# Optimization experiments

Hardware: AMD Instinct MI355X
Metric: run time of the kernel (lower is better)

The kernel has to match this reference:

```python
import jax, jax.numpy as jnp
import numpy as np

UNITS = 512
EPS = 1e-6

def setup_inputs() -> dict:
    key = jax.random.key(0)
    x = jax.random.normal(key, (262144, UNITS), dtype=jnp.float32)
    return {"x": x}

def reference(x):
    d = x.shape[1]
    # Gram matrix with diagonal jitter: [d, d]
    g = x.T @ x + jnp.eye(d, dtype=x.dtype) * EPS
    L = jnp.linalg.cholesky(g)  # lower triangular [d, d]
    # inv(L) via triangular solve (same math as tf.linalg.inv on L)
    L_inv = jax.scipy.linalg.solve_triangular(L, jnp.eye(d, dtype=x.dtype), lower=True)
    ortho_weights = L_inv.T * jnp.sqrt(jnp.float32(UNITS))
    return x @ ortho_weights
```

## Files before the change

### kernel.cpp

```cpp
#include <hip/hip_runtime.h>


#define EPSJ 1e-6f
#define SQRTD 22.627416997969522f

typedef short bf16x8 __attribute__((ext_vector_type(8)));
typedef float f32x4 __attribute__((ext_vector_type(4)));

__device__ __forceinline__ unsigned short f2bf(float f) {
  unsigned u = __float_as_uint(f);
  unsigned r = u + 0x7fffu + ((u >> 16) & 1u);
  return (unsigned short)(r >> 16);
}

__device__ __forceinline__ int swz(int row, int slot) {
  return slot ^ ((row ^ (row >> 3)) & 7);
}

__device__ __forceinline__ float wred(float s) {
  s += __shfl_xor(s, 1);  s += __shfl_xor(s, 2);  s += __shfl_xor(s, 4);
  s += __shfl_xor(s, 8);  s += __shfl_xor(s, 16); s += __shfl_xor(s, 32);
  return s;
}

__global__ __launch_bounds__(512, 2) void gram_partial(
    const float* __restrict__ X, float* __restrict__ part, int nchunk) {
  __shared__ unsigned short As[256 * 64];
  __shared__ unsigned short Bs[256 * 64];
  const int b = blockIdx.x;
  const int pos = b % 3;
  const int chunk = b / 3;
  const int CR = 262144 / nchunk;
  const long r0 = (long)chunk * CR;
  const int ca = (pos == 1) ? 256 : 0;
  const int cb = (pos == 0) ? 0 : 256;
  const bool diag = (pos != 2);
  const int t = threadIdx.x, lane = t & 63, w = t >> 6;
  const int wr = w >> 2, wc = w & 3;

  f32x4 acc[8][4];
  const f32x4 zf = {0.f, 0.f, 0.f, 0.f};
  #pragma unroll
  for (int a = 0; a < 8; ++a)
    #pragma unroll
    for (int bb = 0; bb < 4; ++bb) acc[a][bb] = zf;

  const int c_oct = t & 31, msub = t >> 5;

  for (int ks = 0; ks < CR; ks += 64) {
    #pragma unroll
    for (int it = 0; it < 4; ++it) {
      int m = msub + 16 * it;
      long row = r0 + ks + m;
      const float4* sa = (const float4*)(X + row * 512 + ca + c_oct * 8);
      float4 a0 = sa[0], a1 = sa[1];
      {
        float v[8] = {a0.x, a0.y, a0.z, a0.w, a1.x, a1.y, a1.z, a1.w};
        #pragma unroll
        for (int s = 0; s < 8; ++s) {
          int c = c_oct * 8 + s;
          int off = c * 128 + ((2 * m) ^ (((c ^ (c >> 3)) & 7) << 4));
          *(unsigned short*)((char*)As + off) = f2bf(v[s]);
        }
      }
      if (!diag) {
        const float4* sb = (const float4*)(X + row * 512 + cb + c_oct * 8);
        float4 b0 = sb[0], b1 = sb[1];
        float v[8] = {b0.x, b0.y, b0.z, b0.w, b1.x, b1.y, b1.z, b1.w};
        #pragma unroll
        for (int s = 0; s < 8; ++s) {
          int c = c_oct * 8 + s;
          int off = c * 128 + ((2 * m) ^ (((c ^ (c >> 3)) & 7) << 4));
          *(unsigned short*)((char*)Bs + off) = f2bf(v[s]);
        }
      }
    }
    __syncthreads();
    const unsigned short* Bp = diag ? As : Bs;
    #pragma unroll
    for (int kk = 0; kk < 2; ++kk) {
      bf16x8 af[8], bfr[4];
      #pragma unroll
      for (int fm = 0; fm < 8; ++fm) {
        int row = wr * 128 + fm * 16 + (lane & 15);
        int slot = swz(row, kk * 4 + (lane >> 4));
        af[fm] = *(const bf16x8*)((const char*)As + row * 128 + slot * 16);
      }
      #pragma unroll
      for (int fn = 0; fn < 4; ++fn) {
        int row = wc * 64 + fn * 16 + (lane & 15);
        int slot = swz(row, kk * 4 + (lane >> 4));
        bfr[fn] = *(const bf16x8*)((const char*)Bp + row * 128 + slot * 16);
      }
      #pragma unroll
      for (int fm = 0; fm < 8; ++fm)
        #pragma unroll
        for (int fn = 0; fn < 4; ++fn)
          acc[fm][fn] = __builtin_amdgcn_mfma_f32_16x16x32_bf16(
              af[fm], bfr[fn], acc[fm][fn], 0, 0, 0);
    }
    __syncthreads();
  }
  float* out = part + (long)b * 65536;
  #pragma unroll
  for (int fm = 0; fm < 8; ++fm)
    #pragma unroll
    for (int fn = 0; fn < 4; ++fn)
      #pragma unroll
      for (int j = 0; j < 4; ++j) {
        int i  = wr * 128 + fm * 16 + (lane >> 4) * 4 + j;
        int jj = wc * 64 + fn * 16 + (lane & 15);
        out[i * 256 + jj] = acc[fm][fn][j];
      }
}

__global__ void gram_reduce(const float* __restrict__ part,
                            float* __restrict__ G, int nchunk) {
  int idx = blockIdx.x * 256 + threadIdx.x;
  int pos = idx >> 16;
  int e = idx & 65535;
  float s = 0.f;
  for (int ch = 0; ch < nchunk; ++ch)
    s += part[(long)(ch * 3 + pos) * 65536 + e];
  int i = e >> 8, j = e & 255;
  if (pos == 0) {
    G[i * 512 + j] = s;
  } else if (pos == 1) {
    G[(256 + i) * 512 + 256 + j] = s;
  } else {
    G[i * 512 + 256 + j] = s;
    G[(256 + j) * 512 + i] = s;
  }
}

__global__ void chol_diag(float* __restrict__ G, int c0) {
  __shared__ float P[128][129];
  int t = threadIdx.x;
  for (int idx = t; idx < 128 * 128; idx += 512) {
    int i = idx >> 7, j = idx & 127;
    float v = G[(long)(c0 + i) * 512 + c0 + j];
    if (i == j) v += EPSJ;
    P[i][j] = v;
  }
  __syncthreads();
  int lane = t & 63, w = t >> 6;
  for (int sp = 0; sp < 4; ++sp) {
    int b0 = sp * 32;
    if (w == 0) {
      float r[32];
      #pragma unroll
      for (int k = 0; k < 32; ++k) r[k] = (lane < 32) ? P[b0 + lane][b0 + k] : 0.f;
      #pragma unroll
      for (int j = 0; j < 32; ++j) {
        float d = sqrtf(__shfl(r[j], j));
        if (lane == j) r[j] = d;
        else if (lane > j && lane < 32) r[j] = r[j] / d;
        float rj = r[j];
        #pragma unroll
        for (int k = j + 1; k < 32; ++k) {
          float Lkj = __shfl(rj, k);
          if (lane > j && lane < 32) r[k] -= rj * Lkj;
        }
      }
      #pragma unroll
      for (int k = 0; k < 32; ++k) if (lane < 32) P[b0 + lane][b0 + k] = r[k];
    }
    __syncthreads();
    int nb = 128 - (b0 + 32);
    if (nb > 0) {
      if (t < nb) {
        int rr = b0 + 32 + t;
        float x[32];
        #pragma unroll
        for (int j = 0; j < 32; ++j) x[j] = P[rr][b0 + j];
        #pragma unroll
        for (int j = 0; j < 32; ++j) {
          float xj = x[j] / P[b0 + j][b0 + j];
          x[j] = xj;
          #pragma unroll
          for (int k2 = j + 1; k2 < 32; ++k2) x[k2] -= xj * P[b0 + k2][b0 + j];
        }
        #pragma unroll
        for (int j = 0; j < 32; ++j) P[rr][b0 + j] = x[j];
      }
      __syncthreads();
      int total = nb * nb;
      for (int idx = t; idx < total; idx += 512) {
        int i = b0 + 32 + idx / nb, k = b0 + 32 + idx % nb;
        float s = P[i][k];
        #pragma unroll
        for (int j = 0; j < 32; ++j) s -= P[i][b0 + j] * P[k][b0 + j];
        P[i][k] = s;
      }
      __syncthreads();
    }
  }
  for (int idx = t; idx < 128 * 128; idx += 512) {
    int i = idx >> 7, j = idx & 127;
    G[(long)(c0 + i) * 512 + c0 + j] = P[i][j];
  }
}

__global__ void chol_solve(float* __restrict__ G, int p) {
  int c0 = 128 * p;
  int row0 = c0 + 128;
  int w = threadIdx.x >> 6, lane = threadIdx.x & 63;
  long r = row0 + blockIdx.x * 4 + w;
  float x[2];
  x[0] = G[r * 512 + c0 + lane];
  x[1] = G[r * 512 + c0 + 64 + lane];
  #pragma unroll
  for (int q = 0; q < 2; ++q) {
    for (int ii = 0; ii < 64; ++ii) {
      int i = q * 64 + ii;
      const float* Lrow = G + (long)(c0 + i) * 512 + c0;
      float s = 0.f;
      if (q == 1) s += x[0] * Lrow[lane];
      s += (lane < ii) ? x[q] * Lrow[q * 64 + lane] : 0.f;
      s = wred(s);
      float ai = __shfl(x[q], ii);
      float xi = (ai - s) / Lrow[i];
      if (lane == ii) x[q] = xi;
    }
  }
  G[r * 512 + c0 + lane] = x[0];
  G[r * 512 + c0 + 64 + lane] = x[1];
}

__global__ void chol_syrk(float* __restrict__ G, int t0) {
  int id = blockIdx.x;
  int ti = 0;
  while ((ti + 1) * (ti + 2) / 2 <= id) ++ti;
  int tj = id - ti * (ti + 1) / 2;
  __shared__ float As2[64][130], Bs2[64][130];
  int t = threadIdx.x;
  int c0 = t0 - 128;
  for (int idx = t; idx < 64 * 128; idx += 256) {
    int i = idx >> 7, j = idx & 127;
    As2[i][j] = G[(long)(t0 + 64 * ti + i) * 512 + c0 + j];
    Bs2[i][j] = G[(long)(t0 + 64 * tj + i) * 512 + c0 + j];
  }
  __syncthreads();
  int tr = (t >> 4) * 4, tc = (t & 15) * 4;
  float cacc[4][4];
  #pragma unroll
  for (int u = 0; u < 4; ++u)
    #pragma unroll
    for (int v = 0; v < 4; ++v) cacc[u][v] = 0.f;
  for (int k = 0; k < 128; ++k) {
    float a4[4], b4[4];
    #pragma unroll
    for (int u = 0; u < 4; ++u) { a4[u] = As2[tr + u][k]; b4[u] = Bs2[tc + u][k]; }
    #pragma unroll
    for (int u = 0; u < 4; ++u)
      #pragma unroll
      for (int v = 0; v < 4; ++v) cacc[u][v] += a4[u] * b4[v];
  }
  #pragma unroll
  for (int u = 0; u < 4; ++u)
    #pragma unroll
    for (int v = 0; v < 4; ++v)
      G[(long)(t0 + 64 * ti + tr + u) * 512 + t0 + 64 * tj + tc + v] -= cacc[u][v];
}

__global__ void tri_inv(const float* __restrict__ G,
                        unsigned short* __restrict__ Wt) {
  int w = threadIdx.x >> 6, lane = threadIdx.x & 63;
  int c = blockIdx.x * 4 + w;
  float v8[8];
  #pragma unroll
  for (int q = 0; q < 8; ++q) v8[q] = 0.f;
  #pragma unroll
  for (int q = 0; q < 8; ++q) {
    for (int ii = 0; ii < 64; ++ii) {
      int i = q * 64 + ii;
      const float* Lrow = G + (long)i * 512;
      float s = 0.f;
      #pragma unroll
      for (int qq = 0; qq < 8; ++qq) {
        if (qq < q) s += v8[qq] * Lrow[qq * 64 + lane];
      }
      s += (lane < ii) ? v8[q] * Lrow[q * 64 + lane] : 0.f;
      s = wred(s);
      float xi = (((i == c) ? 1.f : 0.f) - s) / Lrow[i];
      if (lane == ii) v8[q] = xi;
    }
  }
  #pragma unroll
  for (int q = 0; q < 8; ++q) {
    int i = q * 64 + lane;
    Wt[(long)i * 512 + c] = f2bf(SQRTD * v8[q]);
  }
}

__global__ __launch_bounds__(256) void ymm(const float* __restrict__ X,
                                           const unsigned short* __restrict__ Wt,
                                           float* __restrict__ Y) {
  __shared__ unsigned short As[128 * 64];
  __shared__ unsigned short Bs[128 * 64];
  const int t = threadIdx.x, lane = t & 63, w = t >> 6;
  const long m0 = (long)blockIdx.x * 128;
  const int n0 = blockIdx.y * 128;
  const int wm = (w >> 1) * 64, wn = (w & 1) * 64;
  f32x4 acc[4][4];
  const f32x4 zf = {0.f, 0.f, 0.f, 0.f};
  #pragma unroll
  for (int a = 0; a < 4; ++a)
    #pragma unroll
    for (int bq = 0; bq < 4; ++bq) acc[a][bq] = zf;
  const int ko = t & 7, mrow = t >> 3;

  for (int k0 = 0; k0 < 512; k0 += 64) {
    #pragma unroll
    for (int it = 0; it < 4; ++it) {
      int m = mrow + 32 * it;
      const float4* src = (const float4*)(X + (m0 + m) * 512 + k0 + ko * 8);
      float4 f0 = src[0], f1 = src[1];
      unsigned p0 = (unsigned)f2bf(f0.x) | ((unsigned)f2bf(f0.y) << 16);
      unsigned p1 = (unsigned)f2bf(f0.z) | ((unsigned)f2bf(f0.w) << 16);
      unsigned p2 = (unsigned)f2bf(f1.x) | ((unsigned)f2bf(f1.y) << 16);
      unsigned p3 = (unsigned)f2bf(f1.z) | ((unsigned)f2bf(f1.w) << 16);
      int slot = swz(m, ko);
      *(uint4*)((char*)As + m * 128 + slot * 16) = make_uint4(p0, p1, p2, p3);
    }
    #pragma unroll
    for (int it = 0; it < 4; ++it) {
      int n = mrow + 32 * it;
      uint4 raw = *(const uint4*)(Wt + (long)(n0 + n) * 512 + k0 + ko * 8);
      int slot = swz(n, ko);
      *(uint4*)((char*)Bs + n * 128 + slot * 16) = raw;
    }
    __syncthreads();
    #pragma unroll
    for (int kk = 0; kk < 2; ++kk) {
      bf16x8 af[4], bfr[4];
      #pragma unroll
      for (int fm = 0; fm < 4; ++fm) {
        int row = wm + fm * 16 + (lane & 15);
        af[fm] = *(const bf16x8*)((const char*)As + row * 128 +
                                  swz(row, kk * 4 + (lane >> 4)) * 16);
      }
      #pragma unroll
      for (int fn = 0; fn < 4; ++fn) {
        int row = wn + fn * 16 + (lane & 15);
        bfr[fn] = *(const bf16x8*)((const char*)Bs + row * 128 +
                                   swz(row, kk * 4 + (lane >> 4)) * 16);
      }
      #pragma unroll
      for (int fm = 0; fm < 4; ++fm)
        #pragma unroll
        for (int fn = 0; fn < 4; ++fn)
          acc[fm][fn] = __builtin_amdgcn_mfma_f32_16x16x32_bf16(
              af[fm], bfr[fn], acc[fm][fn], 0, 0, 0);
    }
    __syncthreads();
  }
  #pragma unroll
  for (int fm = 0; fm < 4; ++fm)
    #pragma unroll
    for (int fn = 0; fn < 4; ++fn)
      #pragma unroll
      for (int j = 0; j < 4; ++j) {
        long row = m0 + wm + fm * 16 + (lane >> 4) * 4 + j;
        int col = n0 + wn + fn * 16 + (lane & 15);
        Y[row * 512 + col] = acc[fm][fn][j];
      }
}

extern "C" void kernel_launch(void* const* d_in, const int* in_sizes, int n_in,
                              void* d_out, int out_size, void* d_ws, size_t ws_size,
                              hipStream_t stream) {
  const float* X = (const float*)d_in[0];
  float* Y = (float*)d_out;
  char* ws = (char*)d_ws;
  float* G = (float*)ws;
  unsigned short* Wt = (unsigned short*)(ws + (1 << 20));
  float* part = (float*)(ws + (1 << 20) + (1 << 19));
  size_t fixed = (size_t)(1 << 20) + (1 << 19);
  int nchunk = 64;
  while (nchunk > 1 && fixed + (size_t)nchunk * 3 * 65536 * 4 > ws_size)
    nchunk >>= 1;

  gram_partial<<<3 * nchunk, 512, 0, stream>>>(X, part, nchunk);
  gram_reduce<<<768, 256, 0, stream>>>(part, G, nchunk);
  for (int p = 0; p < 4; ++p) {
    chol_diag<<<1, 512, 0, stream>>>(G, 128 * p);
    if (p < 3) {
      int row0 = 128 * (p + 1);
      chol_solve<<<(512 - row0) / 4, 256, 0, stream>>>(G, p);
      int nt = (512 - row0) / 64;
      chol_syrk<<<nt * (nt + 1) / 2, 256, 0, stream>>>(G, row0);
    }
  }
  tri_inv<<<128, 256, 0, stream>>>(G, Wt);
  ymm<<<dim3(2048, 4), 256, 0, stream>>>(X, Wt, Y);
}
```

Baseline: 1.672 ms.

## Pre-convert X to bf16 once and reuse it for Gram and output GEMM

Adds a pass that converts X to bf16 in workspace, so the Gram kernel and the final GEMM both read half-size bf16 instead of fp32 and convert on the fly. The new output GEMM uses direct global-to-LDS loads with double buffering, and tri_inv writes the weights in a pre-swizzled layout to match. The Gram split changes to 85 chunks. This costs an extra 512MB of workspace traffic for the conversion, and the fast path only runs when the workspace is large enough; otherwise the old path is used.

```diff
diff --git a/kernel.cpp b/kernel.cpp
--- a/kernel.cpp
+++ b/kernel.cpp
@@ -23,7 +23,119 @@
   return s;
 }
 
-__global__ __launch_bounds__(512, 2) void gram_partial(
+#define GLOAD16(g, l)                                                         \
+  __builtin_amdgcn_global_load_lds(                                           \
+      (const __attribute__((address_space(1))) void*)(g),                     \
+      (__attribute__((address_space(3))) void*)(l), 16, 0, 0)
+
+__global__ void convert_bf(const float* __restrict__ X,
+                           unsigned short* __restrict__ Xbf) {
+  long idx = (long)blockIdx.x * blockDim.x + threadIdx.x;
+  const long stride = (long)gridDim.x * blockDim.x;
+  const long nch = 134217728 / 8;
+  for (long i = idx; i < nch; i += stride) {
+    float4 f0 = ((const float4*)X)[i * 2];
+    float4 f1 = ((const float4*)X)[i * 2 + 1];
+    uint4 o;
+    o.x = (unsigned)f2bf(f0.x) | ((unsigned)f2bf(f0.y) << 16);
+    o.y = (unsigned)f2bf(f0.z) | ((unsigned)f2bf(f0.w) << 16);
+    o.z = (unsigned)f2bf(f1.x) | ((unsigned)f2bf(f1.y) << 16);
+    o.w = (unsigned)f2bf(f1.z) | ((unsigned)f2bf(f1.w) << 16);
+    ((uint4*)Xbf)[i] = o;
+  }
+}
+
+__device__ __forceinline__ void stage_pack(const unsigned short* __restrict__ src,
+                                           unsigned short* dst, int c0, int k) {
+  uint4 a = *(const uint4*)src;
+  uint4 b = *(const uint4*)(src + 512);
+  unsigned av[4] = {a.x, a.y, a.z, a.w}, bv[4] = {b.x, b.y, b.z, b.w};
+  int k7 = (k & 7) * 2, khi = k >> 3;
+  #pragma unroll
+  for (int j = 0; j < 4; ++j) {
+    int cA = c0 + 2 * j, cB = cA + 1;
+    unsigned lo = (av[j] & 0xFFFFu) | (bv[j] << 16);
+    unsigned hi = (av[j] >> 16) | (bv[j] & 0xFFFF0000u);
+    int slA = khi ^ ((cA ^ (cA >> 3)) & 7);
+    int slB = khi ^ ((cB ^ (cB >> 3)) & 7);
+    *(unsigned*)((char*)dst + cA * 128 + slA * 16 + k7) = lo;
+    *(unsigned*)((char*)dst + cB * 128 + slB * 16 + k7) = hi;
+  }
+}
+
+__global__ __launch_bounds__(512, 2) void gram_bf(
+    const unsigned short* __restrict__ Xbf, float* __restrict__ part,
+    int nchunk) {
+  __shared__ unsigned short As[256 * 64];
+  __shared__ unsigned short Bs[256 * 64];
+  const int b = blockIdx.x, pos = b % 3, chunk = b / 3;
+  const int s0 = (int)((long)4096 * chunk / nchunk);
+  const int s1 = (int)((long)4096 * (chunk + 1) / nchunk);
+  const int ca = (pos == 1) ? 256 : 0;
+  const int cb2 = (pos == 0) ? 0 : 256;
+  const bool diag = (pos != 2);
+  const int t = threadIdx.x, lane = t & 63, w = t >> 6;
+  const int wr = w >> 2, wc = w & 3;
+
+  f32x4 acc[8][4];
+  const f32x4 zf = {0.f, 0.f, 0.f, 0.f};
+  #pragma unroll
+  for (int a = 0; a < 8; ++a)
+    #pragma unroll
+    for (int bb = 0; bb < 4; ++bb) acc[a][bb] = zf;
+
+  const int c0 = (t & 31) * 8;
+  const int kp = t >> 5;
+
+  for (int ks = s0; ks < s1; ++ks) {
+    long rb = (long)ks * 64;
+    #pragma unroll
+    for (int it = 0; it < 2; ++it) {
+      int k = it * 32 + kp * 2;
+      long r = rb + k;
+      stage_pack(Xbf + r * 512 + ca + c0, As, c0, k);
+      if (!diag) stage_pack(Xbf + r * 512 + cb2 + c0, Bs, c0, k);
+    }
+    __syncthreads();
+    const unsigned short* Bp = diag ? As : Bs;
+    #pragma unroll
+    for (int kk = 0; kk < 2; ++kk) {
+      bf16x8 af[8], bfr[4];
+      #pragma unroll
+      for (int fm = 0; fm < 8; ++fm) {
+        int row = wr * 128 + fm * 16 + (lane & 15);
+        int slot = swz(row, kk * 4 + (lane >> 4));
+        af[fm] = *(const bf16x8*)((const char*)As + row * 128 + slot * 16);
+      }
+      #pragma unroll
+      for (int fn = 0; fn < 4; ++fn) {
+        int row = wc * 64 + fn * 16 + (lane & 15);
+        int slot = swz(row, kk * 4 + (lane >> 4));
+        bfr[fn] = *(const bf16x8*)((const char*)Bp + row * 128 + slot * 16);
+      }
+      #pragma unroll
+      for (int fm = 0; fm < 8; ++fm)
+        #pragma unroll
+        for (int fn = 0; fn < 4; ++fn)
+          acc[fm][fn] = __builtin_amdgcn_mfma_f32_16x16x32_bf16(
+              af[fm], bfr[fn], acc[fm][fn], 0, 0, 0);
+    }
+    __syncthreads();
+  }
+  float* out = part + (long)b * 65536;
+  #pragma unroll
+  for (int fm = 0; fm < 8; ++fm)
+    #pragma unroll
+    for (int fn = 0; fn < 4; ++fn)
+      #pragma unroll
+      for (int j = 0; j < 4; ++j) {
+        int i  = wr * 128 + fm * 16 + (lane >> 4) * 4 + j;
+        int jj = wc * 64 + fn * 16 + (lane & 15);
+        out[i * 256 + jj] = acc[fm][fn][j];
+      }
+}
+
+__global__ __launch_bounds__(512, 2) void gram_f32(
     const float* __restrict__ X, float* __restrict__ part, int nchunk) {
   __shared__ unsigned short As[256 * 64];
   __shared__ unsigned short Bs[256 * 64];
@@ -263,6 +375,7 @@
       G[(long)(t0 + 64 * ti + tr + u) * 512 + t0 + 64 * tj + tc + v] -= cacc[u][v];
 }
 
+template <bool SWZ>
 __global__ void tri_inv(const float* __restrict__ G,
                         unsigned short* __restrict__ Wt) {
   int w = threadIdx.x >> 6, lane = threadIdx.x & 63;
@@ -286,16 +399,104 @@
       if (lane == ii) v8[q] = xi;
     }
   }
-  #pragma unroll
-  for (int q = 0; q < 8; ++q) {
-    int i = q * 64 + lane;
-    Wt[(long)i * 512 + c] = f2bf(SQRTD * v8[q]);
-  }
-}
-
-__global__ __launch_bounds__(256) void ymm(const float* __restrict__ X,
-                                           const unsigned short* __restrict__ Wt,
-                                           float* __restrict__ Y) {
+  if (SWZ) {
+    int ko = (c >> 3) & 7, jj = c & 7, cb = c & ~63;
+    #pragma unroll
+    for (int q = 0; q < 8; ++q) {
+      int n = q * 64 + lane;
+      int sl = ko ^ ((n ^ (n >> 3)) & 7);
+      Wt[(long)n * 512 + cb + sl * 8 + jj] = f2bf(SQRTD * v8[q]);
+    }
+  } else {
+    #pragma unroll
+    for (int q = 0; q < 8; ++q) {
+      int i = q * 64 + lane;
+      Wt[(long)i * 512 + c] = f2bf(SQRTD * v8[q]);
+    }
+  }
+}
+
+__global__ __launch_bounds__(256, 2) void ymm2(
+    const unsigned short* __restrict__ Xbf,
+    const unsigned short* __restrict__ Wt, float* __restrict__ Y) {
+  __shared__ unsigned short As[2][128 * 64];
+  __shared__ unsigned short Bs[2][128 * 64];
+  const int t = threadIdx.x, lane = t & 63, w = t >> 6;
+  const long m0 = (long)blockIdx.y * 128;
+  const int n0 = blockIdx.x * 128;
+  const int wm = (w >> 1) * 64, wn = (w & 1) * 64;
+  const int lrow = lane >> 3, lslot = lane & 7;
+  f32x4 acc[4][4];
+  const f32x4 zf = {0.f, 0.f, 0.f, 0.f};
+  #pragma unroll
+  for (int a = 0; a < 4; ++a)
+    #pragma unroll
+    for (int bq = 0; bq < 4; ++bq) acc[a][bq] = zf;
+
+  auto stage = [&](int buf, int k0) {
+    #pragma unroll
+    for (int j = 0; j < 4; ++j) {
+      int row = (w * 4 + j) * 8 + lrow;
+      const unsigned short* sA =
+          Xbf + (m0 + row) * 512 + k0 + swz(row, lslot) * 8;
+      const unsigned short* sB =
+          Wt + (long)(n0 + row) * 512 + k0 + lslot * 8;
+      GLOAD16(sA, &As[buf][(w * 4 + j) * 512]);
+      GLOAD16(sB, &Bs[buf][(w * 4 + j) * 512]);
+    }
+  };
+  auto compute = [&](int buf) {
+    #pragma unroll
+    for (int kk = 0; kk < 2; ++kk) {
+      bf16x8 af[4], bfr[4];
+      #pragma unroll
+      for (int fm = 0; fm < 4; ++fm) {
+        int row = wm + fm * 16 + (lane & 15);
+        af[fm] = *(const bf16x8*)((const char*)As[buf] + row * 128 +
+                                  swz(row, kk * 4 + (lane >> 4)) * 16);
+      }
+      #pragma unroll
+      for (int fn = 0; fn < 4; ++fn) {
+        int row = wn + fn * 16 + (lane & 15);
+        bfr[fn] = *(const bf16x8*)((const char*)Bs[buf] + row * 128 +
+                                   swz(row, kk * 4 + (lane >> 4)) * 16);
+      }
+      #pragma unroll
+      for (int fm = 0; fm < 4; ++fm)
+        #pragma unroll
+        for (int fn = 0; fn < 4; ++fn)
+          acc[fm][fn] = __builtin_amdgcn_mfma_f32_16x16x32_bf16(
+              af[fm], bfr[fn], acc[fm][fn], 0, 0, 0);
+    }
+  };
+
+  stage(0, 0);
+  __syncthreads();
+  int cur = 0;
+  #pragma unroll 1
+  for (int kt = 0; kt < 7; ++kt) {
+    stage(cur ^ 1, (kt + 1) * 64);
+    compute(cur);
+    __syncthreads();
+    cur ^= 1;
+  }
+  compute(cur);
+
+  #pragma unroll
+  for (int fm = 0; fm < 4; ++fm)
+    #pragma unroll
+    for (int fn = 0; fn < 4; ++fn)
+      #pragma unroll
+      for (int j = 0; j < 4; ++j) {
+        long row = m0 + wm + fm * 16 + (lane >> 4) * 4 + j;
+        int col = n0 + wn + fn * 16 + (lane & 15);
+        Y[row * 512 + col] = acc[fm][fn][j];
+      }
+}
+
+__global__ __launch_bounds__(256) void ymm_v1(const float* __restrict__ X,
+                                              const unsigned short* __restrict__ Wt,
+                                              float* __restrict__ Y) {
   __shared__ unsigned short As[128 * 64];
   __shared__ unsigned short Bs[128 * 64];
   const int t = threadIdx.x, lane = t & 63, w = t >> 6;
@@ -367,6 +568,18 @@
       }
 }
 
+static void chol_chain(float* G, hipStream_t stream) {
+  for (int p = 0; p < 4; ++p) {
+    chol_diag<<<1, 512, 0, stream>>>(G, 128 * p);
+    if (p < 3) {
+      int row0 = 128 * (p + 1);
+      chol_solve<<<(512 - row0) / 4, 256, 0, stream>>>(G, p);
+      int nt = (512 - row0) / 64;
+      chol_syrk<<<nt * (nt + 1) / 2, 256, 0, stream>>>(G, row0);
+    }
+  }
+}
+
 extern "C" void kernel_launch(void* const* d_in, const int* in_sizes, int n_in,
                               void* d_out, int out_size, void* d_ws, size_t ws_size,
                               hipStream_t stream) {
@@ -375,23 +588,32 @@
   char* ws = (char*)d_ws;
   float* G = (float*)ws;
   unsigned short* Wt = (unsigned short*)(ws + (1 << 20));
-  float* part = (float*)(ws + (1 << 20) + (1 << 19));
-  size_t fixed = (size_t)(1 << 20) + (1 << 19);
-  int nchunk = 64;
-  while (nchunk > 1 && fixed + (size_t)nchunk * 3 * 65536 * 4 > ws_size)
-    nchunk >>= 1;
-
-  gram_partial<<<3 * nchunk, 512, 0, stream>>>(X, part, nchunk);
-  gram_reduce<<<768, 256, 0, stream>>>(part, G, nchunk);
-  for (int p = 0; p < 4; ++p) {
-    chol_diag<<<1, 512, 0, stream>>>(G, 128 * p);
-    if (p < 3) {
-      int row0 = 128 * (p + 1);
-      chol_solve<<<(512 - row0) / 4, 256, 0, stream>>>(G, p);
-      int nt = (512 - row0) / 64;
-      chol_syrk<<<nt * (nt + 1) / 2, 256, 0, stream>>>(G, row0);
-    }
-  }
-  tri_inv<<<128, 256, 0, stream>>>(G, Wt);
-  ymm<<<dim3(2048, 4), 256, 0, stream>>>(X, Wt, Y);
-}
+  char* wsp = ws + (1 << 20) + (1 << 19);
+
+  const int NCH_FAST = 85;
+  size_t part_bytes = (size_t)NCH_FAST * 3 * 65536 * 4;
+  size_t xbf_off = (size_t)(1 << 20) + (1 << 19) + part_bytes;
+  size_t need = xbf_off + (size_t)134217728 * 2;
+
+  if (ws_size >= need) {
+    float* part = (float*)wsp;
+    unsigned short* Xbf = (unsigned short*)(ws + xbf_off);
+    convert_bf<<<2048, 256, 0, stream>>>(X, Xbf);
+    gram_bf<<<3 * NCH_FAST, 512, 0, stream>>>(Xbf, part, NCH_FAST);
+    gram_reduce<<<768, 256, 0, stream>>>(part, G, NCH_FAST);
+    chol_chain(G, stream);
+    tri_inv<true><<<128, 256, 0, stream>>>(G, Wt);
+    ymm2<<<dim3(4, 2048), 256, 0, stream>>>(Xbf, Wt, Y);
+  } else {
+    float* part = (float*)wsp;
+    size_t fixed = (size_t)(1 << 20) + (1 << 19);
+    int nchunk = 64;
+    while (nchunk > 1 && fixed + (size_t)nchunk * 3 * 65536 * 4 > ws_size)
+      nchunk >>= 1;
+    gram_f32<<<3 * nchunk, 512, 0, stream>>>(X, part, nchunk);
+    gram_reduce<<<768, 256, 0, stream>>>(part, G, nchunk);
+    chol_chain(G, stream);
+    tri_inv<false><<<128, 256, 0, stream>>>(G, Wt);
+    ymm_v1<<<dim3(2048, 4), 256, 0, stream>>>(X, Wt, Y);
+  }
+}
```

Measured after the change: 1.464 ms. -12.4%, faster.
